# Kernel tuning notes

Measured on AMD Instinct MI355X. Metric: run time of the kernel, lower is better.

## Reference

```python
import jax, jax.numpy as jnp
import numpy as np

N, C = 1000000, 64
K = 64


def setup_inputs() -> dict:
    key = jax.random.key(0)
    k1, k2 = jax.random.split(key)
    point_feat = jax.random.normal(k1, (N, C), dtype=jnp.float32)
    # points in [-1, 1)^3 so floor indices land in [0, K)
    points = jax.random.uniform(k2, (N, 3), dtype=jnp.float32) * 2.0 - 1.0
    return {"point_feat": point_feat, "points": points, "k": K}


def reference(point_feat, points, k):
    # voxel index per point: floor((p+1)*k/2) dot [k^2, k, 1]
    p = (points + 1.0) * (k / 2.0)
    pi = jnp.floor(p).astype(jnp.int32)
    pi = jnp.clip(pi, 0, k - 1)  # guard exact boundary p == 1.0
    ks = jnp.array([k * k, k, 1], dtype=jnp.int32)
    pidx = pi @ ks  # (N,) flat cell index in [0, k^3)
    num_cells = k ** 3
    # scatter-mean: sum features per cell, divide by per-cell point count
    sums = jax.ops.segment_sum(point_feat, pidx, num_segments=num_cells)  # (k^3, C)
    counts = jax.ops.segment_sum(jnp.ones((pidx.shape[0],), dtype=point_feat.dtype),
                                 pidx, num_segments=num_cells)  # (k^3,)
    denom = jnp.where(counts > 0, counts, 1.0)
    out = sums / denom[:, None]
    return out.reshape((k, k, k, point_feat.shape[1]))
```

## Files before the change

kernel.cpp:

```cpp
#include <hip/hip_runtime.h>


#define KGRID  64
#define NCH    64
#define NCELLS (KGRID * KGRID * KGRID)
#define CAP    15
#define SPILLCAP 8192

__device__ __forceinline__ int cell_of(float px, float py, float pz) {
    int ix = min(max((int)floorf((px + 1.0f) * 32.0f), 0), KGRID - 1);
    int iy = min(max((int)floorf((py + 1.0f) * 32.0f), 0), KGRID - 1);
    int iz = min(max((int)floorf((pz + 1.0f) * 32.0f), 0), KGRID - 1);
    return (ix << 12) | (iy << 6) | iz;
}

__device__ __forceinline__ void fadd4(float4& a, const float4& b) {
    a.x += b.x; a.y += b.y; a.z += b.z; a.w += b.w;
}

__global__ __launch_bounds__(256) void assign_pts(
    const float* __restrict__ pts,
    int* __restrict__ rec,
    int* __restrict__ nspill,
    int* __restrict__ spill,
    int n)
{
    int t = blockIdx.x * blockDim.x + threadIdx.x;
    int p0 = t * 4;
    if (p0 >= n) return;
    if (p0 + 4 <= n) {
        const float4* p4 = (const float4*)(pts + (size_t)p0 * 3);
        float4 a = p4[0], b = p4[1], c = p4[2];
        int cid[4];
        cid[0] = cell_of(a.x, a.y, a.z);
        cid[1] = cell_of(a.w, b.x, b.y);
        cid[2] = cell_of(b.z, b.w, c.x);
        cid[3] = cell_of(c.y, c.z, c.w);
        #pragma unroll
        for (int i = 0; i < 4; ++i) {
            int* base = rec + ((size_t)cid[i] << 4);
            int slot = __hip_atomic_fetch_add(base, 1, __ATOMIC_RELAXED,
                                              __HIP_MEMORY_SCOPE_AGENT);
            if (slot < CAP) {
                base[1 + slot] = p0 + i;
            } else {
                int s = atomicAdd(nspill, 1);
                if (s < SPILLCAP) { spill[2 * s] = cid[i]; spill[2 * s + 1] = p0 + i; }
            }
        }
    } else {
        for (int p = p0; p < n; ++p) {
            int c = cell_of(pts[3 * p], pts[3 * p + 1], pts[3 * p + 2]);
            int* base = rec + ((size_t)c << 4);
            int slot = __hip_atomic_fetch_add(base, 1, __ATOMIC_RELAXED,
                                              __HIP_MEMORY_SCOPE_AGENT);
            if (slot < CAP) {
                base[1 + slot] = p;
            } else {
                int s = atomicAdd(nspill, 1);
                if (s < SPILLCAP) { spill[2 * s] = c; spill[2 * s + 1] = p; }
            }
        }
    }
}

__global__ __launch_bounds__(256) void reduce_bucket(
    const float4* __restrict__ feat4,
    const int* __restrict__ rec,
    const int* __restrict__ nspill,
    const int* __restrict__ spill,
    float4* __restrict__ out4)
{
    int lane = threadIdx.x & 63;
    int wave = (int)((blockIdx.x * blockDim.x + threadIdx.x) >> 6);
    int grp  = lane >> 4;
    int ch4  = lane & 15;
    int cell = wave * 4 + grp;

    const int4* r4 = (const int4*)(rec + ((size_t)cell << 4));
    int4 r0 = r4[0];
    int4 r1 = r4[1];
    int4 r2 = r4[2];
    int4 r3 = r4[3];

    int cnt = r0.x;
    int len = min(cnt, CAP);
    int e0 = (len > 0) ? r0.y : 0;
    int e1 = (len > 1) ? r0.z : e0;
    int e2 = (len > 2) ? r0.w : e0;
    int e3 = (len > 3) ? r1.x : e0;
    int e4 = (len > 4) ? r1.y : e0;
    int e5 = (len > 5) ? r1.z : e0;
    int e6 = (len > 6) ? r1.w : e0;
    int e7 = (len > 7) ? r2.x : e0;

    const float4* fb = feat4 + ch4;
    float4 f0 = fb[(size_t)e0 * 16];
    float4 f1 = fb[(size_t)e1 * 16];
    float4 f2 = fb[(size_t)e2 * 16];
    float4 f3 = fb[(size_t)e3 * 16];
    float4 f4 = fb[(size_t)e4 * 16];
    float4 f5 = fb[(size_t)e5 * 16];
    float4 f6 = fb[(size_t)e6 * 16];
    float4 f7 = fb[(size_t)e7 * 16];

    float4 acc = make_float4(0.f, 0.f, 0.f, 0.f);
    if (len > 0) fadd4(acc, f0);
    if (len > 1) fadd4(acc, f1);
    if (len > 2) fadd4(acc, f2);
    if (len > 3) fadd4(acc, f3);
    if (len > 4) fadd4(acc, f4);
    if (len > 5) fadd4(acc, f5);
    if (len > 6) fadd4(acc, f6);
    if (len > 7) fadd4(acc, f7);

    if (len > 8) {
        fadd4(acc, fb[(size_t)r2.y * 16]);
        if (len > 9)  fadd4(acc, fb[(size_t)r2.z * 16]);
        if (len > 10) fadd4(acc, fb[(size_t)r2.w * 16]);
        if (len > 11) fadd4(acc, fb[(size_t)r3.x * 16]);
        if (len > 12) fadd4(acc, fb[(size_t)r3.y * 16]);
        if (len > 13) fadd4(acc, fb[(size_t)r3.z * 16]);
        if (len > 14) fadd4(acc, fb[(size_t)r3.w * 16]);
    }
    if (cnt > CAP) {
        int ns = min(*nspill, SPILLCAP);
        for (int s = 0; s < ns; ++s) {
            if (spill[2 * s] == cell) fadd4(acc, fb[(size_t)spill[2 * s + 1] * 16]);
        }
    }
    float inv = 1.0f / (float)max(cnt, 1);
    acc.x *= inv; acc.y *= inv; acc.z *= inv; acc.w *= inv;

    out4[(size_t)wave * 64 + lane] = acc;
}

extern "C" void kernel_launch(void* const* d_in, const int* in_sizes, int n_in,
                              void* d_out, int out_size, void* d_ws, size_t ws_size,
                              hipStream_t stream)
{
    const float* feat = (const float*)d_in[0];
    const float* pts  = (const float*)d_in[1];
    float* out = (float*)d_out;

    const int n = in_sizes[0] / NCH;

    int* rec    = (int*)d_ws;
    int* nspill = rec + (size_t)NCELLS * 16;
    int* spill  = nspill + 4;

    hipMemsetAsync(rec, 0, ((size_t)NCELLS * 16 + 4) * sizeof(int), stream);

    int t4 = (n + 3) / 4;
    int pblocks = (t4 + 255) / 256;
    assign_pts<<<pblocks, 256, 0, stream>>>(pts, rec, nspill, spill, n);

    reduce_bucket<<<NCELLS / 16, 256, 0, stream>>>(
        (const float4*)feat, rec, nspill, spill, (float4*)out);
}
```

Measured before the change: 419.5 us.

## Convert features to fp16 during assignment and gather half-precision in reduction

After: 461.0 us. +9.9%, slower.

```diff
diff --git a/kernel.cpp b/kernel.cpp
--- a/kernel.cpp
+++ b/kernel.cpp
@@ -1,4 +1,5 @@
 #include <hip/hip_runtime.h>
+#include <hip/hip_fp16.h>
 
 
 #define KGRID  64
@@ -7,6 +8,10 @@
 #define CAP    15
 #define SPILLCAP 8192
 
+typedef float f32x4 __attribute__((ext_vector_type(4)));
+
+union HU { unsigned u; __half2 h; };
+
 __device__ __forceinline__ int cell_of(float px, float py, float pz) {
     int ix = min(max((int)floorf((px + 1.0f) * 32.0f), 0), KGRID - 1);
     int iy = min(max((int)floorf((py + 1.0f) * 32.0f), 0), KGRID - 1);
@@ -18,16 +23,24 @@
     a.x += b.x; a.y += b.y; a.z += b.z; a.w += b.w;
 }
 
+__device__ __forceinline__ void hacc(float4& a, uint2 q) {
+    HU u0, u1; u0.u = q.x; u1.u = q.y;
+    float2 f0 = __half22float2(u0.h);
+    float2 f1 = __half22float2(u1.h);
+    a.x += f0.x; a.y += f0.y; a.z += f1.x; a.w += f1.y;
+}
+
 __global__ __launch_bounds__(256) void assign_pts(
     const float* __restrict__ pts,
+    const f32x4* __restrict__ feat4,
+    uint2* __restrict__ feat16,
     int* __restrict__ rec,
     int* __restrict__ nspill,
     int* __restrict__ spill,
-    int n)
+    int n, int nthreads, int do_convert)
 {
     int t = blockIdx.x * blockDim.x + threadIdx.x;
     int p0 = t * 4;
-    if (p0 >= n) return;
     if (p0 + 4 <= n) {
         const float4* p4 = (const float4*)(pts + (size_t)p0 * 3);
         float4 a = p4[0], b = p4[1], c = p4[2];
@@ -48,7 +61,7 @@
                 if (s < SPILLCAP) { spill[2 * s] = cid[i]; spill[2 * s + 1] = p0 + i; }
             }
         }
-    } else {
+    } else if (p0 < n) {
         for (int p = p0; p < n; ++p) {
             int c = cell_of(pts[3 * p], pts[3 * p + 1], pts[3 * p + 2]);
             int* base = rec + ((size_t)c << 4);
@@ -62,14 +75,26 @@
             }
         }
     }
-}
-
-__global__ __launch_bounds__(256) void reduce_bucket(
-    const float4* __restrict__ feat4,
+
+    if (do_convert) {
+        int total = n * (NCH / 4);
+        for (int idx = t; idx < total; idx += nthreads) {
+            f32x4 v = __builtin_nontemporal_load(feat4 + idx);
+            HU u0, u1;
+            u0.h = __floats2half2_rn(v.x, v.y);
+            u1.h = __floats2half2_rn(v.z, v.w);
+            uint2 q; q.x = u0.u; q.y = u1.u;
+            feat16[idx] = q;
+        }
+    }
+}
+
+__global__ __launch_bounds__(256) void reduce_bucket16(
+    const uint2* __restrict__ feat16,
     const int* __restrict__ rec,
     const int* __restrict__ nspill,
     const int* __restrict__ spill,
-    float4* __restrict__ out4)
+    f32x4* __restrict__ out4)
 {
     int lane = threadIdx.x & 63;
     int wave = (int)((blockIdx.x * blockDim.x + threadIdx.x) >> 6);
@@ -94,6 +119,77 @@
     int e6 = (len > 6) ? r1.w : e0;
     int e7 = (len > 7) ? r2.x : e0;
 
+    const uint2* fb = feat16 + ch4;
+    uint2 q0 = fb[(size_t)e0 * 16];
+    uint2 q1 = fb[(size_t)e1 * 16];
+    uint2 q2 = fb[(size_t)e2 * 16];
+    uint2 q3 = fb[(size_t)e3 * 16];
+    uint2 q4 = fb[(size_t)e4 * 16];
+    uint2 q5 = fb[(size_t)e5 * 16];
+    uint2 q6 = fb[(size_t)e6 * 16];
+    uint2 q7 = fb[(size_t)e7 * 16];
+
+    float4 acc = make_float4(0.f, 0.f, 0.f, 0.f);
+    if (len > 0) hacc(acc, q0);
+    if (len > 1) hacc(acc, q1);
+    if (len > 2) hacc(acc, q2);
+    if (len > 3) hacc(acc, q3);
+    if (len > 4) hacc(acc, q4);
+    if (len > 5) hacc(acc, q5);
+    if (len > 6) hacc(acc, q6);
+    if (len > 7) hacc(acc, q7);
+
+    if (len > 8) {
+        hacc(acc, fb[(size_t)r2.y * 16]);
+        if (len > 9)  hacc(acc, fb[(size_t)r2.z * 16]);
+        if (len > 10) hacc(acc, fb[(size_t)r2.w * 16]);
+        if (len > 11) hacc(acc, fb[(size_t)r3.x * 16]);
+        if (len > 12) hacc(acc, fb[(size_t)r3.y * 16]);
+        if (len > 13) hacc(acc, fb[(size_t)r3.z * 16]);
+        if (len > 14) hacc(acc, fb[(size_t)r3.w * 16]);
+    }
+    if (cnt > CAP) {
+        int ns = min(*nspill, SPILLCAP);
+        for (int s = 0; s < ns; ++s) {
+            if (spill[2 * s] == cell) hacc(acc, fb[(size_t)spill[2 * s + 1] * 16]);
+        }
+    }
+    float inv = 1.0f / (float)max(cnt, 1);
+    f32x4 o;
+    o.x = acc.x * inv; o.y = acc.y * inv; o.z = acc.z * inv; o.w = acc.w * inv;
+    __builtin_nontemporal_store(o, out4 + (size_t)wave * 64 + lane);
+}
+
+__global__ __launch_bounds__(256) void reduce_bucket32(
+    const float4* __restrict__ feat4,
+    const int* __restrict__ rec,
+    const int* __restrict__ nspill,
+    const int* __restrict__ spill,
+    float4* __restrict__ out4)
+{
+    int lane = threadIdx.x & 63;
+    int wave = (int)((blockIdx.x * blockDim.x + threadIdx.x) >> 6);
+    int grp  = lane >> 4;
+    int ch4  = lane & 15;
+    int cell = wave * 4 + grp;
+
+    const int4* r4 = (const int4*)(rec + ((size_t)cell << 4));
+    int4 r0 = r4[0];
+    int4 r1 = r4[1];
+    int4 r2 = r4[2];
+    int4 r3 = r4[3];
+
+    int cnt = r0.x;
+    int len = min(cnt, CAP);
+    int e0 = (len > 0) ? r0.y : 0;
+    int e1 = (len > 1) ? r0.z : e0;
+    int e2 = (len > 2) ? r0.w : e0;
+    int e3 = (len > 3) ? r1.x : e0;
+    int e4 = (len > 4) ? r1.y : e0;
+    int e5 = (len > 5) ? r1.z : e0;
+    int e6 = (len > 6) ? r1.w : e0;
+    int e7 = (len > 7) ? r2.x : e0;
+
     const float4* fb = feat4 + ch4;
     float4 f0 = fb[(size_t)e0 * 16];
     float4 f1 = fb[(size_t)e1 * 16];
@@ -131,7 +227,6 @@
     }
     float inv = 1.0f / (float)max(cnt, 1);
     acc.x *= inv; acc.y *= inv; acc.z *= inv; acc.w *= inv;
-
     out4[(size_t)wave * 64 + lane] = acc;
 }
 
@@ -148,13 +243,25 @@
     int* rec    = (int*)d_ws;
     int* nspill = rec + (size_t)NCELLS * 16;
     int* spill  = nspill + 4;
+    uint2* feat16 = (uint2*)(spill + 2 * SPILLCAP);
+
+    size_t base_bytes = ((size_t)NCELLS * 16 + 4 + 2 * SPILLCAP) * sizeof(int);
+    size_t need16     = base_bytes + (size_t)n * 128;
+    int use16 = (ws_size >= need16) ? 1 : 0;
 
     hipMemsetAsync(rec, 0, ((size_t)NCELLS * 16 + 4) * sizeof(int), stream);
 
     int t4 = (n + 3) / 4;
     int pblocks = (t4 + 255) / 256;
-    assign_pts<<<pblocks, 256, 0, stream>>>(pts, rec, nspill, spill, n);
-
-    reduce_bucket<<<NCELLS / 16, 256, 0, stream>>>(
-        (const float4*)feat, rec, nspill, spill, (float4*)out);
-}
+    int nthreads = pblocks * 256;
+    assign_pts<<<pblocks, 256, 0, stream>>>(
+        pts, (const f32x4*)feat, feat16, rec, nspill, spill, n, nthreads, use16);
+
+    if (use16) {
+        reduce_bucket16<<<NCELLS / 16, 256, 0, stream>>>(
+            (const uint2*)feat16, rec, nspill, spill, (f32x4*)out);
+    } else {
+        reduce_bucket32<<<NCELLS / 16, 256, 0, stream>>>(
+            (const float4*)feat, rec, nspill, spill, (float4*)out);
+    }
+}
```
